# Kernel optimization log

Measured on AMD Instinct MI355X. Metric: run time of the kernel, lower is better.

Reference implementation:

```python
import jax, jax.numpy as jnp
import numpy as np

# Production-scale dims (see shape_source)
B, H, W, C = 8, 64, 64, 256
KH, KW = 3, 3
BASES = 16
FILTERS = 256


def setup_inputs() -> dict:
    key = jax.random.key(0)
    k1, k2, k3, k4 = jax.random.split(key, 4)
    x = jax.random.normal(k1, (B, H, W, C), dtype=jnp.float32)
    # P: channel-mixing matrix [C, C] (initialized to identity in build, then assigned)
    P = jax.random.normal(k2, (C, C), dtype=jnp.float32) * 0.05
    # Q: per-channel basis kernels [C, kh, kw, bases]
    Q = jax.random.normal(k3, (C, KH, KW, BASES), dtype=jnp.float32) * 0.1
    # S: basis-combination weights [C, bases, filters]
    S = jax.random.normal(k4, (C, BASES, FILTERS), dtype=jnp.float32) * 0.05
    return {"x": x, "P": P, "Q": Q, "S": S}


def reference(x, P, Q, S):
    # --- Step 1: channel mixing (the vectorized_map over calculate_J) ---
    # J[o] = sum_c x[..., c] * P[o, c]  ->  one GEMM over channels
    mixed = jnp.einsum('bhwc,oc->bhwo', x, P)  # [B,H,W,C]

    C_ = P.shape[0]
    kh, kw, bases = Q.shape[1], Q.shape[2], Q.shape[3]

    # --- Step 2: per-channel conv with `bases` basis kernels (the map_fn loop) ---
    # Expressed as ONE grouped (depthwise-style) conv: group c produces outputs
    # [c*bases : (c+1)*bases], matching kernel flatten order (c, b).
    rhs = jnp.transpose(Q, (1, 2, 0, 3)).reshape(kh, kw, 1, C_ * bases)  # HWIO
    dw = jax.lax.conv_general_dilated(
        mixed, rhs, window_strides=(1, 1), padding='VALID',
        dimension_numbers=('NHWC', 'HWIO', 'NHWC'),
        feature_group_count=C_,
    )  # [B, H-kh+1, W-kw+1, C*bases], channel index k = c*bases + b

    b, h, w, _ = dw.shape
    # tau in the original: [B, h, w, bases, C]
    tau = dw.reshape(b, h, w, C_, bases).transpose(0, 1, 2, 4, 3)

    # --- Step 3: basis-weighted combination (the vectorized_map over calculate_O) ---
    # Original flattens tau row-major over (bases, C) and S[:, :, f] row-major over
    # (C, bases), then does an elementwise dot over the flat axis. Replicate exactly.
    Tflat = tau.reshape(b, h, w, bases * C_)          # flat index k = b_idx*C + c
    Sflat = S.reshape(C_ * bases, S.shape[-1])        # flat index k = c*bases + b_idx
    O = jnp.einsum('bhwk,kf->bhwf', Tflat, Sflat)     # [B, h, w, filters]
    return O
```

## Files before the change

### kernel.cpp

```cpp
#include <hip/hip_runtime.h>
#include <hip/hip_bf16.h>

typedef __attribute__((ext_vector_type(4))) float f32x4;
typedef __attribute__((ext_vector_type(8))) short bf16x8;

#define M_TOT 30752

__device__ __forceinline__ unsigned short f2bf(float f) {
  unsigned int u = __float_as_uint(f);
  u = u + 0x7FFF + ((u >> 16) & 1);
  return (unsigned short)(u >> 16);
}

__device__ __forceinline__ void gload16(const void* g, void* l) {
  __builtin_amdgcn_global_load_lds((const __attribute__((address_space(1))) unsigned int*)g,
                                   (__attribute__((address_space(3))) unsigned int*)l,
                                   16, 0, 0);
}

__global__ __launch_bounds__(256) void prep1(const float* __restrict__ x,
                                             const float* __restrict__ Q,
                                             const float* __restrict__ S,
                                             unsigned short* __restrict__ xb,
                                             float* __restrict__ Keff) {
  const int bid = blockIdx.x;
  const int t = threadIdx.x;

  if (bid < 4096) {
    int i = bid * 256 + t;
    const f32x4* xp = (const f32x4*)x;
    f32x4 a = xp[2 * i];
    f32x4 b = xp[2 * i + 1];
    bf16x8 o;
    o[0] = (short)f2bf(a[0]); o[1] = (short)f2bf(a[1]);
    o[2] = (short)f2bf(a[2]); o[3] = (short)f2bf(a[3]);
    o[4] = (short)f2bf(b[0]); o[5] = (short)f2bf(b[1]);
    o[6] = (short)f2bf(b[2]); o[7] = (short)f2bf(b[3]);
    ((bf16x8*)xb)[i] = o;
    return;
  }

  const int o = bid - 4096;
  float s[16];
  const float* sp = S + (o >> 4) * 4096 + (o & 15) * 256 + t;
#pragma unroll
  for (int bi = 0; bi < 16; ++bi) s[bi] = sp[bi * 65536];
  const float* qp = Q + o * 144;
#pragma unroll
  for (int kk = 0; kk < 9; ++kk) {
    float a = 0.f;
#pragma unroll
    for (int bi = 0; bi < 16; ++bi) a = fmaf(qp[kk * 16 + bi], s[bi], a);
    Keff[(o * 9 + kk) * 256 + t] = a;
  }
}

__global__ __launch_bounds__(256) void k2t_k(const float* __restrict__ P,
                                             const float* __restrict__ Keff,
                                             unsigned short* __restrict__ K2t) {
  const int kk = blockIdx.x >> 6;
  const int f0 = (blockIdx.x & 63) * 4;
  const int ci = threadIdx.x;
  float acc[4] = {0.f, 0.f, 0.f, 0.f};
#pragma unroll 8
  for (int o = 0; o < 256; ++o) {
    float pv = P[o * 256 + ci];
    const float* ke = Keff + (o * 9 + kk) * 256 + f0;
    acc[0] = fmaf(pv, ke[0], acc[0]);
    acc[1] = fmaf(pv, ke[1], acc[1]);
    acc[2] = fmaf(pv, ke[2], acc[2]);
    acc[3] = fmaf(pv, ke[3], acc[3]);
  }
#pragma unroll
  for (int j = 0; j < 4; ++j)
    K2t[kk * 65536 + (f0 + j) * 256 + ci] = f2bf(acc[j]);
}

__global__ __launch_bounds__(512, 2) void conv_gemm(const unsigned short* __restrict__ xb,
                                                    const unsigned short* __restrict__ K2t,
                                                    float* __restrict__ out) {
  __shared__ __attribute__((aligned(16))) char smem[147456];
  unsigned short* const A0 = (unsigned short*)(smem);
  unsigned short* const B0 = (unsigned short*)(smem + 16384);
  unsigned short* const A1 = (unsigned short*)(smem + 49152);
  unsigned short* const B1 = (unsigned short*)(smem + 65536);
  unsigned short* const A2 = (unsigned short*)(smem + 98304);
  unsigned short* const B2 = (unsigned short*)(smem + 114688);
  float* const red = (float*)smem;

  const int tid = threadIdx.x;
  const int lane = tid & 63;
  const int sk = tid >> 8;
  const int wn = (tid >> 6) & 3;
  const int m0 = blockIdx.x * 128;

  const int rl = lane & 15;
  const int kg = lane >> 4;

  const int s_src = ((tid & 3) ^ ((tid >> 3) & 3)) * 8;
  int gAa;
  {
    int m = m0 + (tid >> 2); if (m >= M_TOT) m = M_TOT - 1;
    int b = m / 3844; int rem = m - b * 3844;
    int h = rem / 62; int w = rem - h * 62;
    gAa = ((b * 64 + h) * 64 + w) * 256 + s_src;
  }
  const int fB0 = (tid >> 2) * 256 + s_src;
  const int fB1 = ((tid >> 2) + 128) * 256 + s_src;

  f32x4 zero = {0.f, 0.f, 0.f, 0.f};
  f32x4 acc[8][4];
#pragma unroll
  for (int i = 0; i < 8; ++i)
#pragma unroll
    for (int j = 0; j < 4; ++j) acc[i][j] = zero;

  const int slotr = (kg ^ ((rl >> 1) & 3)) * 16;
  const int aoff = sk * 8192 + rl * 64 + slotr;
  const int boff = sk * 16384 + (wn * 64 + rl) * 64 + slotr;

#define STAGE(t, bufA, bufB)                                                   \
  {                                                                            \
    int kk_ = (t) >> 2, cb_ = (t) & 3;                                         \
    int kh_ = kk_ / 3, kw_ = kk_ - kh_ * 3;                                    \
    int offA_ = kh_ * 16384 + kw_ * 256 + cb_ * 64;                            \
    int offB_ = kk_ * 65536 + cb_ * 64;                                        \
    gload16(xb + gAa + offA_,       &bufA[tid * 8]);                           \
    gload16(xb + gAa + offA_ + 32,  &bufA[(tid + 512) * 8]);                   \
    gload16(K2t + offB_ + fB0,      &bufB[tid * 8]);                           \
    gload16(K2t + offB_ + fB1,      &bufB[(tid + 512) * 8]);                   \
    gload16(K2t + offB_ + fB0 + 32, &bufB[(tid + 1024) * 8]);                  \
    gload16(K2t + offB_ + fB1 + 32, &bufB[(tid + 1536) * 8]);                  \
  }

#define STEP(t, cA, cB, nA, nB)                                                \
  {                                                                            \
    if ((t) == 35) asm volatile("s_waitcnt vmcnt(0)" ::: "memory");            \
    else           asm volatile("s_waitcnt vmcnt(6)" ::: "memory");            \
    __builtin_amdgcn_sched_barrier(0);                                         \
    __builtin_amdgcn_s_barrier();                                              \
    __builtin_amdgcn_sched_barrier(0);                                         \
    if ((t) < 34) { STAGE((t) + 2, nA, nB); }                                  \
    bf16x8 af[8], bfr[4];                                                      \
    _Pragma("unroll")                                                          \
    for (int mi = 0; mi < 8; ++mi)                                             \
      af[mi] = *(const bf16x8*)((const char*)(cA) + aoff + mi * 1024);         \
    _Pragma("unroll")                                                          \
    for (int ni = 0; ni < 4; ++ni)                                             \
      bfr[ni] = *(const bf16x8*)((const char*)(cB) + boff + ni * 1024);        \
    __builtin_amdgcn_s_setprio(1);                                             \
    _Pragma("unroll")                                                          \
    for (int mi = 0; mi < 8; ++mi)                                             \
      _Pragma("unroll")                                                        \
      for (int ni = 0; ni < 4; ++ni)                                           \
        acc[mi][ni] = __builtin_amdgcn_mfma_f32_16x16x32_bf16(                 \
            af[mi], bfr[ni], acc[mi][ni], 0, 0, 0);                            \
    __builtin_amdgcn_s_setprio(0);                                             \
  }

  STAGE(0, A0, B0);
  STAGE(1, A1, B1);

  for (int tt = 0; tt < 12; ++tt) {
    int t0 = tt * 3;
    STEP(t0,     A0, B0, A2, B2);
    STEP(t0 + 1, A1, B1, A0, B0);
    STEP(t0 + 2, A2, B2, A1, B1);
  }

  __syncthreads();

#pragma unroll
  for (int round = 0; round < 2; ++round) {
    if (sk == 1) {
#pragma unroll
      for (int mc = 0; mc < 4; ++mc)
#pragma unroll
        for (int ni = 0; ni < 4; ++ni)
          *(f32x4*)((char*)red + (((wn * 4 + mc) * 4 + ni) * 64 + lane) * 16) =
              acc[round * 4 + mc][ni];
    }
    __syncthreads();
    if (sk == 0) {
#pragma unroll
      for (int mc = 0; mc < 4; ++mc) {
        int mi = round * 4 + mc;
        int mb = m0 + mi * 16 + kg * 4;
#pragma unroll
        for (int ni = 0; ni < 4; ++ni) {
          f32x4 o = *(f32x4*)((char*)red + (((wn * 4 + mc) * 4 + ni) * 64 + lane) * 16);
          o += acc[mi][ni];
          int f = wn * 64 + ni * 16 + rl;
#pragma unroll
          for (int r = 0; r < 4; ++r) {
            int m = mb + r;
            if (m < M_TOT) out[m * 256 + f] = o[r];
          }
        }
      }
    }
    __syncthreads();
  }
#undef STAGE
#undef STEP
}

extern "C" void kernel_launch(void* const* d_in, const int* in_sizes, int n_in,
                              void* d_out, int out_size, void* d_ws, size_t ws_size,
                              hipStream_t stream) {
  const float* x = (const float*)d_in[0];
  const float* P = (const float*)d_in[1];
  const float* Q = (const float*)d_in[2];
  const float* S = (const float*)d_in[3];
  float* out = (float*)d_out;

  char* ws = (char*)d_ws;
  unsigned short* xb   = (unsigned short*)ws;
  unsigned short* K2t  = (unsigned short*)(ws + 16777216);
  float*          Keff = (float*)(ws + 16777216 + 1179648);

  prep1<<<4096 + 256, 256, 0, stream>>>(x, Q, S, xb, Keff);
  k2t_k<<<576, 256, 0, stream>>>(P, Keff, K2t);
  conv_gemm<<<241, 512, 0, stream>>>(xb, K2t, out);
}
```

Baseline: 76.27 us.

## Split conv GEMM into 128x128 tiles with double-buffered LDS and XCD-aware block mapping

Reworks the implicit-GEMM conv kernel from 241 blocks of 512 threads, each covering all 256 filters with a triple-buffered 144KB LDS, to 488 blocks of 256 threads. Each block now covers a 128x128 output tile with a double-buffered 64KB LDS. Block IDs are remapped so that pairs of tiles sharing the same M rows land on the same XCD, and the A-fragment loads are interleaved with the MFMAs. The aim is better CU utilisation on a 256-CU part and more resident blocks per CU. The cost is loading each A tile twice, only one stage of prefetch, and an extra barrier per K step.

Measured after the change: 76.92 us. Within noise of the previous version (+0.9%).

```diff
diff --git a/kernel.cpp b/kernel.cpp
--- a/kernel.cpp
+++ b/kernel.cpp
@@ -76,37 +76,41 @@
     K2t[kk * 65536 + (f0 + j) * 256 + ci] = f2bf(acc[j]);
 }
 
-__global__ __launch_bounds__(512, 2) void conv_gemm(const unsigned short* __restrict__ xb,
+__global__ __launch_bounds__(256, 2) void conv_gemm(const unsigned short* __restrict__ xb,
                                                     const unsigned short* __restrict__ K2t,
                                                     float* __restrict__ out) {
-  __shared__ __attribute__((aligned(16))) char smem[147456];
-  unsigned short* const A0 = (unsigned short*)(smem);
-  unsigned short* const B0 = (unsigned short*)(smem + 16384);
-  unsigned short* const A1 = (unsigned short*)(smem + 49152);
-  unsigned short* const B1 = (unsigned short*)(smem + 65536);
-  unsigned short* const A2 = (unsigned short*)(smem + 98304);
-  unsigned short* const B2 = (unsigned short*)(smem + 114688);
-  float* const red = (float*)smem;
+  __shared__ __attribute__((aligned(16))) char smem[65536];
 
   const int tid = threadIdx.x;
   const int lane = tid & 63;
-  const int sk = tid >> 8;
-  const int wn = (tid >> 6) & 3;
-  const int m0 = blockIdx.x * 128;
+  const int wid = tid >> 6;
+  const int sk = wid >> 1;
+  const int wn = wid & 1;
+
+  const int wgid = (blockIdx.x & 7) * 61 + (blockIdx.x >> 3);
+  if (wgid >= 482) return;
+  const int mt = wgid >> 1;
+  const int nt = wgid & 1;
+  const int m0 = mt * 128;
+  const int n0 = nt * 128;
 
   const int rl = lane & 15;
   const int kg = lane >> 4;
 
   const int s_src = ((tid & 3) ^ ((tid >> 3) & 3)) * 8;
-  int gAa;
+  int gA0, gA1;
   {
     int m = m0 + (tid >> 2); if (m >= M_TOT) m = M_TOT - 1;
     int b = m / 3844; int rem = m - b * 3844;
     int h = rem / 62; int w = rem - h * 62;
-    gAa = ((b * 64 + h) * 64 + w) * 256 + s_src;
-  }
-  const int fB0 = (tid >> 2) * 256 + s_src;
-  const int fB1 = ((tid >> 2) + 128) * 256 + s_src;
+    gA0 = ((b * 64 + h) * 64 + w) * 256 + s_src;
+    m = m0 + (tid >> 2) + 64; if (m >= M_TOT) m = M_TOT - 1;
+    b = m / 3844; rem = m - b * 3844;
+    h = rem / 62; w = rem - h * 62;
+    gA1 = ((b * 64 + h) * 64 + w) * 256 + s_src;
+  }
+  const int fB0 = (n0 + (tid >> 2)) * 256 + s_src;
+  const int fB1 = (n0 + (tid >> 2) + 64) * 256 + s_src;
 
   f32x4 zero = {0.f, 0.f, 0.f, 0.f};
   f32x4 acc[8][4];
@@ -117,92 +121,96 @@
 
   const int slotr = (kg ^ ((rl >> 1) & 3)) * 16;
   const int aoff = sk * 8192 + rl * 64 + slotr;
-  const int boff = sk * 16384 + (wn * 64 + rl) * 64 + slotr;
-
-#define STAGE(t, bufA, bufB)                                                   \
+  const int boff = 16384 + sk * 8192 + (wn * 64 + rl) * 64 + slotr;
+
+#define STAGE(t, base)                                                         \
   {                                                                            \
     int kk_ = (t) >> 2, cb_ = (t) & 3;                                         \
     int kh_ = kk_ / 3, kw_ = kk_ - kh_ * 3;                                    \
     int offA_ = kh_ * 16384 + kw_ * 256 + cb_ * 64;                            \
     int offB_ = kk_ * 65536 + cb_ * 64;                                        \
-    gload16(xb + gAa + offA_,       &bufA[tid * 8]);                           \
-    gload16(xb + gAa + offA_ + 32,  &bufA[(tid + 512) * 8]);                   \
-    gload16(K2t + offB_ + fB0,      &bufB[tid * 8]);                           \
-    gload16(K2t + offB_ + fB1,      &bufB[(tid + 512) * 8]);                   \
-    gload16(K2t + offB_ + fB0 + 32, &bufB[(tid + 1024) * 8]);                  \
-    gload16(K2t + offB_ + fB1 + 32, &bufB[(tid + 1536) * 8]);                  \
-  }
-
-#define STEP(t, cA, cB, nA, nB)                                                \
-  {                                                                            \
-    if ((t) == 35) asm volatile("s_waitcnt vmcnt(0)" ::: "memory");            \
-    else           asm volatile("s_waitcnt vmcnt(6)" ::: "memory");            \
-    __builtin_amdgcn_sched_barrier(0);                                         \
-    __builtin_amdgcn_s_barrier();                                              \
-    __builtin_amdgcn_sched_barrier(0);                                         \
-    if ((t) < 34) { STAGE((t) + 2, nA, nB); }                                  \
-    bf16x8 af[8], bfr[4];                                                      \
-    _Pragma("unroll")                                                          \
-    for (int mi = 0; mi < 8; ++mi)                                             \
-      af[mi] = *(const bf16x8*)((const char*)(cA) + aoff + mi * 1024);         \
-    _Pragma("unroll")                                                          \
-    for (int ni = 0; ni < 4; ++ni)                                             \
-      bfr[ni] = *(const bf16x8*)((const char*)(cB) + boff + ni * 1024);        \
-    __builtin_amdgcn_s_setprio(1);                                             \
-    _Pragma("unroll")                                                          \
-    for (int mi = 0; mi < 8; ++mi)                                             \
-      _Pragma("unroll")                                                        \
-      for (int ni = 0; ni < 4; ++ni)                                           \
-        acc[mi][ni] = __builtin_amdgcn_mfma_f32_16x16x32_bf16(                 \
-            af[mi], bfr[ni], acc[mi][ni], 0, 0, 0);                            \
-    __builtin_amdgcn_s_setprio(0);                                             \
-  }
-
-  STAGE(0, A0, B0);
-  STAGE(1, A1, B1);
-
-  for (int tt = 0; tt < 12; ++tt) {
-    int t0 = tt * 3;
-    STEP(t0,     A0, B0, A2, B2);
-    STEP(t0 + 1, A1, B1, A0, B0);
-    STEP(t0 + 2, A2, B2, A1, B1);
-  }
-
+    unsigned short* bA = (unsigned short*)(base);                              \
+    unsigned short* bB = (unsigned short*)((char*)(base) + 16384);             \
+    gload16(xb + gA0 + offA_,      bA + tid * 8);                              \
+    gload16(xb + gA1 + offA_,      bA + (tid + 256) * 8);                      \
+    gload16(xb + gA0 + offA_ + 32, bA + (tid + 512) * 8);                      \
+    gload16(xb + gA1 + offA_ + 32, bA + (tid + 768) * 8);                      \
+    gload16(K2t + offB_ + fB0,      bB + tid * 8);                             \
+    gload16(K2t + offB_ + fB1,      bB + (tid + 256) * 8);                     \
+    gload16(K2t + offB_ + fB0 + 32, bB + (tid + 512) * 8);                     \
+    gload16(K2t + offB_ + fB1 + 32, bB + (tid + 768) * 8);                     \
+  }
+
+  STAGE(0, smem);
+
+  for (int t = 0; t < 36; ++t) {
+    char* cur = smem + (t & 1) * 32768;
+    if (t < 35) STAGE(t + 1, smem + ((t + 1) & 1) * 32768);
+    if (t == 35) asm volatile("s_waitcnt vmcnt(0)" ::: "memory");
+    else         asm volatile("s_waitcnt vmcnt(8)" ::: "memory");
+    __builtin_amdgcn_sched_barrier(0);
+    __builtin_amdgcn_s_barrier();
+    __builtin_amdgcn_sched_barrier(0);
+
+    bf16x8 bfr[4];
+#pragma unroll
+    for (int ni = 0; ni < 4; ++ni)
+      bfr[ni] = *(const bf16x8*)(cur + boff + ni * 1024);
+    bf16x8 a0 = *(const bf16x8*)(cur + aoff);
+    bf16x8 a1 = *(const bf16x8*)(cur + aoff + 1024);
+#pragma unroll
+    for (int j = 0; j < 4; ++j) {
+      bf16x8 a2, a3;
+      if (j < 3) {
+        a2 = *(const bf16x8*)(cur + aoff + (2 * j + 2) * 1024);
+        a3 = *(const bf16x8*)(cur + aoff + (2 * j + 3) * 1024);
+      }
+      __builtin_amdgcn_s_setprio(1);
+#pragma unroll
+      for (int ni = 0; ni < 4; ++ni)
+        acc[2 * j][ni] = __builtin_amdgcn_mfma_f32_16x16x32_bf16(
+            a0, bfr[ni], acc[2 * j][ni], 0, 0, 0);
+#pragma unroll
+      for (int ni = 0; ni < 4; ++ni)
+        acc[2 * j + 1][ni] = __builtin_amdgcn_mfma_f32_16x16x32_bf16(
+            a1, bfr[ni], acc[2 * j + 1][ni], 0, 0, 0);
+      __builtin_amdgcn_s_setprio(0);
+      a0 = a2; a1 = a3;
+    }
+
+    __builtin_amdgcn_sched_barrier(0);
+    __builtin_amdgcn_s_barrier();
+    __builtin_amdgcn_sched_barrier(0);
+  }
+
+  float* red = (float*)smem;
+  if (sk == 1) {
+#pragma unroll
+    for (int mi = 0; mi < 8; ++mi)
+#pragma unroll
+      for (int ni = 0; ni < 4; ++ni)
+        *(f32x4*)((char*)red + (((wn * 8 + mi) * 4 + ni) * 64 + lane) * 16) =
+            acc[mi][ni];
+  }
   __syncthreads();
-
-#pragma unroll
-  for (int round = 0; round < 2; ++round) {
-    if (sk == 1) {
-#pragma unroll
-      for (int mc = 0; mc < 4; ++mc)
-#pragma unroll
-        for (int ni = 0; ni < 4; ++ni)
-          *(f32x4*)((char*)red + (((wn * 4 + mc) * 4 + ni) * 64 + lane) * 16) =
-              acc[round * 4 + mc][ni];
-    }
-    __syncthreads();
-    if (sk == 0) {
-#pragma unroll
-      for (int mc = 0; mc < 4; ++mc) {
-        int mi = round * 4 + mc;
-        int mb = m0 + mi * 16 + kg * 4;
-#pragma unroll
-        for (int ni = 0; ni < 4; ++ni) {
-          f32x4 o = *(f32x4*)((char*)red + (((wn * 4 + mc) * 4 + ni) * 64 + lane) * 16);
-          o += acc[mi][ni];
-          int f = wn * 64 + ni * 16 + rl;
-#pragma unroll
-          for (int r = 0; r < 4; ++r) {
-            int m = mb + r;
-            if (m < M_TOT) out[m * 256 + f] = o[r];
-          }
+  if (sk == 0) {
+#pragma unroll
+    for (int mi = 0; mi < 8; ++mi) {
+      int mb = m0 + mi * 16 + kg * 4;
+#pragma unroll
+      for (int ni = 0; ni < 4; ++ni) {
+        f32x4 o = *(f32x4*)((char*)red + (((wn * 8 + mi) * 4 + ni) * 64 + lane) * 16);
+        o += acc[mi][ni];
+        int f = n0 + wn * 64 + ni * 16 + rl;
+#pragma unroll
+        for (int r = 0; r < 4; ++r) {
+          int m = mb + r;
+          if (m < M_TOT) out[m * 256 + f] = o[r];
         }
       }
     }
-    __syncthreads();
   }
 #undef STAGE
-#undef STEP
 }
 
 extern "C" void kernel_launch(void* const* d_in, const int* in_sizes, int n_in,
@@ -221,5 +229,5 @@
 
   prep1<<<4096 + 256, 256, 0, stream>>>(x, Q, S, xb, Keff);
   k2t_k<<<576, 256, 0, stream>>>(P, Keff, K2t);
-  conv_gemm<<<241, 512, 0, stream>>>(xb, K2t, out);
-}
+  conv_gemm<<<488, 256, 0, stream>>>(xb, K2t, out);
+}
```
